# Kernel tuning notes

Hardware: AMD Instinct MI355X
Metric: run time of the kernel (lower is better)

The kernel has to match this reference:

```python
import jax, jax.numpy as jnp
import numpy as np

NEG = -1e9


def _layer_norm(x, g, b, eps=1e-5):
    m = x.mean(-1, keepdims=True)
    v = x.var(-1, keepdims=True)
    return (x - m) / jnp.sqrt(v + eps) * g + b


def _gat(x, mask, W, a):
    # x: [B,N,Fin], W: [Fin,Fout], a: [2*Fout]
    h = x @ W                                   # [B,N,Fout]
    F = W.shape[1]
    src = h @ a[:F]                             # [B,N]
    dst = h @ a[F:]                             # [B,N]
    e = jax.nn.leaky_relu(src[:, :, None] + dst[:, None, :], 0.2)  # [B,N,N]
    e = jnp.where(mask, e, NEG)
    attn = jax.nn.softmax(e, axis=-1)
    return attn @ h, attn


def _mha(x, mask, Wq, bq, Wk, bk, Wv, bv, Wo, bo, num_heads, head_dim):
    B, N, _ = x.shape
    q = (x @ Wq + bq).reshape(B, N, num_heads, head_dim)
    k = (x @ Wk + bk).reshape(B, N, num_heads, head_dim)
    v = (x @ Wv + bv).reshape(B, N, num_heads, head_dim)
    scores = jnp.einsum('bihd,bjhd->bhij', q, k) / jnp.sqrt(jnp.asarray(head_dim, x.dtype))
    scores = jnp.where(mask[:, None, :, :], scores, NEG)
    attn = jax.nn.softmax(scores, axis=-1)      # [B,H,N,N]
    ctx = jnp.einsum('bhij,bjhd->bihd', attn, v).reshape(B, N, num_heads * head_dim)
    return ctx @ Wo + bo, attn


def setup_inputs() -> dict:
    key = jax.random.key(0)
    ks = jax.random.split(key, 32)
    B, N = 64, 400
    D, Hd, E, H = 400, 256, 128, 4
    hd = Hd // H  # 64
    s = 0.02
    x = jax.random.normal(ks[0], (B, N, D), dtype=jnp.float32)
    adj = (jax.random.uniform(ks[1], (B, N, N)) < 0.15).astype(jnp.float32)
    eye = jnp.eye(N, dtype=jnp.float32)
    adj = jnp.maximum(adj, eye[None])
    def w(k, shape):
        return jax.random.normal(k, shape, dtype=jnp.float32) * s
    return {
        'x': x, 'adj': adj,
        'Wq': w(ks[2], (D, H * hd)), 'bq': jnp.zeros(H * hd),
        'Wk': w(ks[3], (D, H * hd)), 'bk': jnp.zeros(H * hd),
        'Wv': w(ks[4], (D, H * hd)), 'bv': jnp.zeros(H * hd),
        'Wo': w(ks[5], (H * hd, D)), 'bo': jnp.zeros(D),
        'gat1_W': w(ks[6], (D, Hd)), 'gat1_a': w(ks[7], (2 * Hd,)),
        'gat2_W': w(ks[8], (Hd, Hd)), 'gat2_a': w(ks[9], (2 * Hd,)),
        'gat3_W': w(ks[10], (Hd, E)), 'gat3_a': w(ks[11], (2 * E,)),
        'res1_W': w(ks[12], (D, Hd)), 'res1_b': jnp.zeros(Hd),
        'res2_W': w(ks[13], (Hd, Hd)), 'res2_b': jnp.zeros(Hd),
        'res3_W': w(ks[14], (Hd, E)), 'res3_b': jnp.zeros(E),
        'ln1_g': jnp.ones(Hd), 'ln1_b': jnp.zeros(Hd),
        'ln2_g': jnp.ones(Hd), 'ln2_b': jnp.zeros(Hd),
        'ln3_g': jnp.ones(E), 'ln3_b': jnp.zeros(E),
    }


def reference(x, adj, Wq, bq, Wk, bk, Wv, bv, Wo, bo,
              gat1_W, gat1_a, gat2_W, gat2_a, gat3_W, gat3_a,
              res1_W, res1_b, res2_W, res2_b, res3_W, res3_b,
              ln1_g, ln1_b, ln2_g, ln2_b, ln3_g, ln3_b):
    mask = adj > 0
    # eval mode: dropout is identity
    mha_out, _ = _mha(x, mask, Wq, bq, Wk, bk, Wv, bv, Wo, bo, num_heads=4, head_dim=64)
    x = x + mha_out
    g1, attn1 = _gat(x, mask, gat1_W, gat1_a)
    x = jax.nn.elu(_layer_norm(g1 + (x @ res1_W + res1_b), ln1_g, ln1_b))
    g2, attn2 = _gat(x, mask, gat2_W, gat2_a)
    x = jax.nn.elu(_layer_norm(g2 + (x @ res2_W + res2_b), ln2_g, ln2_b))
    g3, attn3 = _gat(x, mask, gat3_W, gat3_a)
    x = _layer_norm(g3 + (x @ res3_W + res3_b), ln3_g, ln3_b)
    return x, (attn1, attn2, attn3)
```

## Files before the change

kernel.cpp:

```cpp
#include <hip/hip_runtime.h>


#define NEGBIG (-1e9f)

typedef __attribute__((ext_vector_type(8))) short bf16x8;
typedef __attribute__((ext_vector_type(4))) float f32x4;

__device__ inline unsigned short f2bf(float f) {
    unsigned u = __builtin_bit_cast(unsigned, f);
    u += 0x7fffu + ((u >> 16) & 1u);
    return (unsigned short)(u >> 16);
}
__device__ inline float bf2f(unsigned short h) {
    unsigned u = ((unsigned)h) << 16;
    return __builtin_bit_cast(float, u);
}

__device__ inline float wave_max(float v) {
#pragma unroll
    for (int off = 32; off >= 1; off >>= 1)
        v = fmaxf(v, __shfl_xor(v, off, 64));
    return v;
}
__device__ inline float wave_sum(float v) {
#pragma unroll
    for (int off = 32; off >= 1; off >>= 1)
        v += __shfl_xor(v, off, 64);
    return v;
}

__global__ __launch_bounds__(256) void transpose_to_bf16(
    const float* __restrict__ in, unsigned short* __restrict__ out,
    int R, int C, long sIn, long sOut)
{
    in  += (long)blockIdx.z * sIn;
    out += (long)blockIdx.z * sOut;
    __shared__ float t[32][33];
    const int r0 = blockIdx.y * 32, c0 = blockIdx.x * 32;
    const int tid = threadIdx.x;

    const int row = tid >> 3, c4 = tid & 7;
    float4 v = make_float4(0.f, 0.f, 0.f, 0.f);
    if (r0 + row < R && c0 + c4 * 4 < C)
        v = *reinterpret_cast<const float4*>(&in[(long)(r0 + row) * C + c0 + c4 * 4]);
    t[row][c4 * 4 + 0] = v.x;
    t[row][c4 * 4 + 1] = v.y;
    t[row][c4 * 4 + 2] = v.z;
    t[row][c4 * 4 + 3] = v.w;
    __syncthreads();

    const int oc = tid >> 3, r4 = tid & 7;
    if (c0 + oc < C && r0 + r4 * 4 < R) {
        ushort4 o;
        o.x = f2bf(t[r4 * 4 + 0][oc]);
        o.y = f2bf(t[r4 * 4 + 1][oc]);
        o.z = f2bf(t[r4 * 4 + 2][oc]);
        o.w = f2bf(t[r4 * 4 + 3][oc]);
        *reinterpret_cast<ushort4*>(&out[(long)(c0 + oc) * R + r0 + r4 * 4]) = o;
    }
}

template<bool BIAS, bool ACCUM, bool RESID>
__global__ __launch_bounds__(256) void gemm_mfma(
    const float* __restrict__ A, const unsigned short* __restrict__ BT,
    const float* __restrict__ bias, const float* __restrict__ resid,
    float* __restrict__ C, int M, int K, int Nc,
    long sA, long sBT, long sC)
{
    const int bz = blockIdx.z;
    A  += (long)bz * sA;
    BT += (long)bz * sBT;
    C  += (long)bz * sC;
    const float* Rp = RESID ? (resid + (long)bz * sC) : nullptr;

    __shared__ short As[64][40];
    __shared__ short Bs[128][40];

    const int tid = threadIdx.x;
    const int lane = tid & 63, wave = tid >> 6;
    const int wm = wave >> 1, wn = wave & 1;
    const int m0 = blockIdx.y * 64, n0 = blockIdx.x * 128;

    f32x4 acc[2][4] = {};

    const int nk = (K + 31) / 32;
    for (int kt = 0; kt < nk; ++kt) {
        const int k0 = kt * 32;
        __syncthreads();
#pragma unroll
        for (int p = 0; p < 2; ++p) {
            const int idx = tid + p * 256;
            const int row = idx >> 3, k4 = idx & 7;
            const int gm = m0 + row, gk = k0 + k4 * 4;
            float4 av = make_float4(0.f, 0.f, 0.f, 0.f);
            if (gm < M && gk < K)
                av = *reinterpret_cast<const float4*>(&A[(long)gm * K + gk]);
            ushort4 h4;
            h4.x = f2bf(av.x); h4.y = f2bf(av.y); h4.z = f2bf(av.z); h4.w = f2bf(av.w);
            *reinterpret_cast<ushort4*>(&As[row][k4 * 4]) = h4;
        }
#pragma unroll
        for (int p = 0; p < 2; ++p) {
            const int idx = tid + p * 256;
            const int n = idx >> 2, k8 = idx & 3;
            const int gn = n0 + n, gk = k0 + k8 * 8;
            uint4 bv = make_uint4(0u, 0u, 0u, 0u);
            if (gn < Nc && gk < K)
                bv = *reinterpret_cast<const uint4*>(&BT[(long)gn * K + gk]);
            *reinterpret_cast<uint4*>(&Bs[n][k8 * 8]) = bv;
        }
        __syncthreads();

        const int fr = lane & 15, fkb = (lane >> 4) * 8;
        bf16x8 a[2], b[4];
#pragma unroll
        for (int i = 0; i < 2; ++i)
            a[i] = *reinterpret_cast<const bf16x8*>(&As[wm * 32 + i * 16 + fr][fkb]);
#pragma unroll
        for (int j = 0; j < 4; ++j)
            b[j] = *reinterpret_cast<const bf16x8*>(&Bs[wn * 64 + j * 16 + fr][fkb]);
#pragma unroll
        for (int i = 0; i < 2; ++i)
#pragma unroll
            for (int j = 0; j < 4; ++j)
                acc[i][j] = __builtin_amdgcn_mfma_f32_16x16x32_bf16(a[i], b[j], acc[i][j], 0, 0, 0);
    }

    const int fr = lane & 15, rg = lane >> 4;
#pragma unroll
    for (int i = 0; i < 2; ++i) {
#pragma unroll
        for (int j = 0; j < 4; ++j) {
#pragma unroll
            for (int r = 0; r < 4; ++r) {
                const int gm = m0 + wm * 32 + i * 16 + rg * 4 + r;
                const int gn = n0 + wn * 64 + j * 16 + fr;
                if (gm < M && gn < Nc) {
                    float v = acc[i][j][r];
                    if (BIAS)  v += bias[gn];
                    if (RESID) v += Rp[(long)gm * Nc + gn];
                    if (ACCUM) v += C[(long)gm * Nc + gn];
                    C[(long)gm * Nc + gn] = v;
                }
            }
        }
    }
}

__global__ __launch_bounds__(256) void mha_flash_mfma(
    const float* __restrict__ q, const float* __restrict__ k,
    const float* __restrict__ v, const float* __restrict__ adj,
    float* __restrict__ ctx)
{
    const int it = blockIdx.x, h = blockIdx.y, b = blockIdx.z;
    const int i0 = it * 64;
    const int tid = threadIdx.x;
    const int lane = tid & 63, w = tid >> 6;
    const int c = lane & 15, g = lane >> 4;

    __shared__ short Qs[64][72];
    __shared__ short Ks[64][72];
    __shared__ short Vt[64][72];
    __shared__ short Ps[64][72];
    __shared__ short Adjs[64][72];

    const long base_q = ((long)b * 400 + i0) * 256 + h * 64;
#pragma unroll
    for (int p = 0; p < 4; ++p) {
        const int idx = tid + p * 256;
        const int r = idx >> 4, c4 = idx & 15;
        float4 qv = make_float4(0.f, 0.f, 0.f, 0.f);
        if (i0 + r < 400)
            qv = *reinterpret_cast<const float4*>(q + base_q + (long)r * 256 + c4 * 4);
        ushort4 h4;
        h4.x = f2bf(qv.x); h4.y = f2bf(qv.y); h4.z = f2bf(qv.z); h4.w = f2bf(qv.w);
        *reinterpret_cast<ushort4*>(&Qs[r][c4 * 4]) = h4;
    }

    f32x4 o[4] = {};
    float m[4] = {-3e38f, -3e38f, -3e38f, -3e38f};
    float l[4] = {0.f, 0.f, 0.f, 0.f};

    for (int jt = 0; jt < 7; ++jt) {
        const int j0 = jt * 64;
        __syncthreads();

        const long base_k = ((long)b * 400 + j0) * 256 + h * 64;
#pragma unroll
        for (int p = 0; p < 4; ++p) {
            const int idx = tid + p * 256;
            const int r = idx >> 4, c4 = idx & 15;
            float4 kv = make_float4(0.f, 0.f, 0.f, 0.f);
            if (j0 + r < 400)
                kv = *reinterpret_cast<const float4*>(k + base_k + (long)r * 256 + c4 * 4);
            ushort4 h4;
            h4.x = f2bf(kv.x); h4.y = f2bf(kv.y); h4.z = f2bf(kv.z); h4.w = f2bf(kv.w);
            *reinterpret_cast<ushort4*>(&Ks[r][c4 * 4]) = h4;

            float4 av = make_float4(0.f, 0.f, 0.f, 0.f);
            if (i0 + r < 400 && j0 + c4 * 4 < 400)
                av = *reinterpret_cast<const float4*>(adj + ((long)b * 400 + i0 + r) * 400 + j0 + c4 * 4);
            ushort4 mb;
            mb.x = f2bf(av.x > 0.f ? 0.f : NEGBIG);
            mb.y = f2bf(av.y > 0.f ? 0.f : NEGBIG);
            mb.z = f2bf(av.z > 0.f ? 0.f : NEGBIG);
            mb.w = f2bf(av.w > 0.f ? 0.f : NEGBIG);
            *reinterpret_cast<ushort4*>(&Adjs[r][c4 * 4]) = mb;
        }
        {
            const int j4 = tid >> 4, d4 = tid & 15;
            float vv[4][4];
#pragma unroll
            for (int t = 0; t < 4; ++t) {
                float4 vl = make_float4(0.f, 0.f, 0.f, 0.f);
                if (j0 + j4 * 4 + t < 400)
                    vl = *reinterpret_cast<const float4*>(v + base_k + (long)(j4 * 4 + t) * 256 + d4 * 4);
                vv[t][0] = vl.x; vv[t][1] = vl.y; vv[t][2] = vl.z; vv[t][3] = vl.w;
            }
#pragma unroll
            for (int u = 0; u < 4; ++u) {
                ushort4 h4;
                h4.x = f2bf(vv[0][u]); h4.y = f2bf(vv[1][u]);
                h4.z = f2bf(vv[2][u]); h4.w = f2bf(vv[3][u]);
                *reinterpret_cast<ushort4*>(&Vt[d4 * 4 + u][j4 * 4]) = h4;
            }
        }
        __syncthreads();

        f32x4 s4[4] = {};
#pragma unroll
        for (int ks = 0; ks < 2; ++ks) {
            const bf16x8 a = *reinterpret_cast<const bf16x8*>(&Qs[w * 16 + c][ks * 32 + g * 8]);
#pragma unroll
            for (int t = 0; t < 4; ++t) {
                const bf16x8 bb = *reinterpret_cast<const bf16x8*>(&Ks[t * 16 + c][ks * 32 + g * 8]);
                s4[t] = __builtin_amdgcn_mfma_f32_16x16x32_bf16(a, bb, s4[t], 0, 0, 0);
            }
        }

        float e[4][4];
        float pmax[4];
#pragma unroll
        for (int reg = 0; reg < 4; ++reg) {
            const int qr = w * 16 + g * 4 + reg;
            float mx = -3e38f;
#pragma unroll
            for (int t = 0; t < 4; ++t) {
                const float ev = s4[t][reg] * 0.125f + bf2f((unsigned short)Adjs[qr][t * 16 + c]);
                e[t][reg] = ev;
                mx = fmaxf(mx, ev);
            }
            pmax[reg] = mx;
        }
#pragma unroll
        for (int reg = 0; reg < 4; ++reg)
#pragma unroll
            for (int off = 1; off <= 8; off <<= 1)
                pmax[reg] = fmaxf(pmax[reg], __shfl_xor(pmax[reg], off, 64));

        float al[4];
#pragma unroll
        for (int reg = 0; reg < 4; ++reg) {
            const float mn = fmaxf(m[reg], pmax[reg]);
            al[reg] = __expf(m[reg] - mn);
            m[reg] = mn;
        }

#pragma unroll
        for (int reg = 0; reg < 4; ++reg) {
            const int qr = w * 16 + g * 4 + reg;
            float psum = 0.f;
#pragma unroll
            for (int t = 0; t < 4; ++t) {
                const float p = __expf(e[t][reg] - m[reg]);
                psum += p;
                Ps[qr][t * 16 + c] = (short)f2bf(p);
            }
            l[reg] = l[reg] * al[reg] + psum;
        }

#pragma unroll
        for (int dt = 0; dt < 4; ++dt)
#pragma unroll
            for (int reg = 0; reg < 4; ++reg)
                o[dt][reg] *= al[reg];

#pragma unroll
        for (int ks = 0; ks < 2; ++ks) {
            const bf16x8 a = *reinterpret_cast<const bf16x8*>(&Ps[w * 16 + c][ks * 32 + g * 8]);
#pragma unroll
            for (int dt = 0; dt < 4; ++dt) {
                const bf16x8 bb = *reinterpret_cast<const bf16x8*>(&Vt[dt * 16 + c][ks * 32 + g * 8]);
                o[dt] = __builtin_amdgcn_mfma_f32_16x16x32_bf16(a, bb, o[dt], 0, 0, 0);
            }
        }
    }

#pragma unroll
    for (int reg = 0; reg < 4; ++reg)
#pragma unroll
        for (int off = 1; off <= 8; off <<= 1)
            l[reg] += __shfl_xor(l[reg], off, 64);

#pragma unroll
    for (int reg = 0; reg < 4; ++reg) {
        const int gi = i0 + w * 16 + g * 4 + reg;
        if (gi < 400) {
            const float inv = 1.f / l[reg];
#pragma unroll
            for (int dt = 0; dt < 4; ++dt)
                ctx[((long)b * 400 + gi) * 256 + h * 64 + dt * 16 + c] = o[dt][reg] * inv;
        }
    }
}

__global__ __launch_bounds__(256) void gat_srcdst(
    const float* __restrict__ h, const float* __restrict__ a,
    float* __restrict__ src, float* __restrict__ dst, int F)
{
    const int row = blockIdx.x * 4 + (threadIdx.x >> 6);
    const int lane = threadIdx.x & 63;
    const float* hp = h + (long)row * F;
    float s = 0.f, d = 0.f;
    for (int f = lane; f < F; f += 64) {
        const float hv = hp[f];
        s += hv * a[f];
        d += hv * a[F + f];
    }
    s = wave_sum(s);
    d = wave_sum(d);
    if (lane == 0) { src[row] = s; dst[row] = d; }
}

__global__ __launch_bounds__(256) void gat_attn(
    const float* __restrict__ src, const float* __restrict__ dst,
    const float* __restrict__ adj, float* __restrict__ attn)
{
    const int row = blockIdx.x * 4 + (threadIdx.x >> 6);
    const int b = row / 400;
    const int lane = threadIdx.x & 63;
    const float si = src[row];
    const float* db = dst + (long)b * 400;
    const float* adjrow = adj + (long)row * 400;

    float e[7];
    float mx = -3.0e38f;
#pragma unroll
    for (int t = 0; t < 7; ++t) {
        const int j = lane + 64 * t;
        float v = -3.0e38f;
        if (j < 400) {
            v = si + db[j];
            v = (v > 0.f) ? v : 0.2f * v;
            if (!(adjrow[j] > 0.f)) v = NEGBIG;
        }
        e[t] = v;
        mx = fmaxf(mx, v);
    }
    mx = wave_max(mx);

    float p[7];
    float sum = 0.f;
#pragma unroll
    for (int t = 0; t < 7; ++t) {
        const int j = lane + 64 * t;
        if (j < 400) {
            p[t] = __expf(e[t] - mx);
            sum += p[t];
        }
    }
    sum = wave_sum(sum);
    const float inv = 1.f / sum;
#pragma unroll
    for (int t = 0; t < 7; ++t) {
        const int j = lane + 64 * t;
        if (j < 400) attn[(long)row * 400 + j] = p[t] * inv;
    }
}

template<int F, bool ELU>
__global__ __launch_bounds__(256) void ln_kernel(
    const float* __restrict__ in, const float* __restrict__ g,
    const float* __restrict__ b, float* __restrict__ out)
{
    const int row = blockIdx.x * 4 + (threadIdx.x >> 6);
    const int lane = threadIdx.x & 63;
    constexpr int PER = F / 64;
    const float* ip = in + (long)row * F;

    float v[PER];
    float s = 0.f;
#pragma unroll
    for (int t = 0; t < PER; ++t) {
        v[t] = ip[lane + 64 * t];
        s += v[t];
    }
    s = wave_sum(s);
    const float mean = s * (1.f / F);
    float vs = 0.f;
#pragma unroll
    for (int t = 0; t < PER; ++t) {
        const float d = v[t] - mean;
        vs += d * d;
    }
    vs = wave_sum(vs);
    const float rstd = rsqrtf(vs * (1.f / F) + 1e-5f);
#pragma unroll
    for (int t = 0; t < PER; ++t) {
        const int col = lane + 64 * t;
        float y = (v[t] - mean) * rstd * g[col] + b[col];
        if (ELU) y = (y > 0.f) ? y : expm1f(y);
        out[(long)row * F + col] = y;
    }
}

extern "C" void kernel_launch(void* const* d_in, const int* in_sizes, int n_in,
                              void* d_out, int out_size, void* d_ws, size_t ws_size,
                              hipStream_t stream) {
    const float* x    = (const float*)d_in[0];
    const float* adj  = (const float*)d_in[1];
    const float* Wq   = (const float*)d_in[2];
    const float* bq   = (const float*)d_in[3];
    const float* Wk   = (const float*)d_in[4];
    const float* bk   = (const float*)d_in[5];
    const float* Wv   = (const float*)d_in[6];
    const float* bv   = (const float*)d_in[7];
    const float* Wo   = (const float*)d_in[8];
    const float* bo   = (const float*)d_in[9];
    const float* g1W  = (const float*)d_in[10];
    const float* g1a  = (const float*)d_in[11];
    const float* g2W  = (const float*)d_in[12];
    const float* g2a  = (const float*)d_in[13];
    const float* g3W  = (const float*)d_in[14];
    const float* g3a  = (const float*)d_in[15];
    const float* r1W  = (const float*)d_in[16];
    const float* r1b  = (const float*)d_in[17];
    const float* r2W  = (const float*)d_in[18];
    const float* r2b  = (const float*)d_in[19];
    const float* r3W  = (const float*)d_in[20];
    const float* r3b  = (const float*)d_in[21];
    const float* ln1g = (const float*)d_in[22];
    const float* ln1b = (const float*)d_in[23];
    const float* ln2g = (const float*)d_in[24];
    const float* ln2b = (const float*)d_in[25];
    const float* ln3g = (const float*)d_in[26];
    const float* ln3b = (const float*)d_in[27];

    float* out_x = (float*)d_out;
    float* attn1 = out_x + 3276800;
    float* attn2 = attn1 + 10240000;
    float* attn3 = attn2 + 10240000;

    float* bufA = (float*)d_ws;
    float* bufB = bufA + 6553600;
    float* bufC = bufB + 6553600;
    float* bufD = bufC + 6553600;
    float* srcb = bufD + 6553600;
    float* dstb = srcb + 25600;
    unsigned short* wT   = (unsigned short*)(dstb + 25600);
    unsigned short* wTq  = wT;
    unsigned short* wTk  = wT + 102400;
    unsigned short* wTv  = wT + 204800;
    unsigned short* wTo  = wT + 307200;
    unsigned short* wTg1 = wT + 409600;
    unsigned short* wTr1 = wT + 512000;
    unsigned short* wTg2 = wT + 614400;
    unsigned short* wTr2 = wT + 679936;
    unsigned short* wTg3 = wT + 745472;
    unsigned short* wTr3 = wT + 778240;
    float* xc = attn1;
    unsigned short* hT1 = (unsigned short*)bufD;
    unsigned short* hT2 = (unsigned short*)bufC;
    unsigned short* hT3 = (unsigned short*)bufD;

    const dim3 blk(256);
    const int M = 25600;

    transpose_to_bf16<<<dim3(8, 13), blk, 0, stream>>>(Wq,  wTq, 400, 256, 0, 0);
    transpose_to_bf16<<<dim3(8, 13), blk, 0, stream>>>(Wk,  wTk, 400, 256, 0, 0);
    transpose_to_bf16<<<dim3(8, 13), blk, 0, stream>>>(Wv,  wTv, 400, 256, 0, 0);
    transpose_to_bf16<<<dim3(13, 8), blk, 0, stream>>>(Wo,  wTo, 256, 400, 0, 0);
    transpose_to_bf16<<<dim3(8, 13), blk, 0, stream>>>(g1W, wTg1, 400, 256, 0, 0);
    transpose_to_bf16<<<dim3(8, 13), blk, 0, stream>>>(r1W, wTr1, 400, 256, 0, 0);
    transpose_to_bf16<<<dim3(8, 8),  blk, 0, stream>>>(g2W, wTg2, 256, 256, 0, 0);
    transpose_to_bf16<<<dim3(8, 8),  blk, 0, stream>>>(r2W, wTr2, 256, 256, 0, 0);
    transpose_to_bf16<<<dim3(4, 8),  blk, 0, stream>>>(g3W, wTg3, 256, 128, 0, 0);
    transpose_to_bf16<<<dim3(4, 8),  blk, 0, stream>>>(r3W, wTr3, 256, 128, 0, 0);

    gemm_mfma<true, false, false><<<dim3(2, 400), blk, 0, stream>>>(x, wTq, bq, nullptr, bufA, M, 400, 256, 0, 0, 0);
    gemm_mfma<true, false, false><<<dim3(2, 400), blk, 0, stream>>>(x, wTk, bk, nullptr, bufB, M, 400, 256, 0, 0, 0);
    gemm_mfma<true, false, false><<<dim3(2, 400), blk, 0, stream>>>(x, wTv, bv, nullptr, bufC, M, 400, 256, 0, 0, 0);
    mha_flash_mfma<<<dim3(7, 4, 64), blk, 0, stream>>>(bufA, bufB, bufC, adj, bufD);
    gemm_mfma<true, false, true><<<dim3(4, 400), blk, 0, stream>>>(bufD, wTo, bo, x, xc, M, 256, 400, 0, 0, 0);

    gemm_mfma<false, false, false><<<dim3(2, 400), blk, 0, stream>>>(xc, wTg1, nullptr, nullptr, bufA, M, 400, 256, 0, 0, 0);
    gemm_mfma<true, false, false><<<dim3(2, 400), blk, 0, stream>>>(xc, wTr1, r1b, nullptr, bufB, M, 400, 256, 0, 0, 0);
    gat_srcdst<<<dim3(6400), blk, 0, stream>>>(bufA, g1a, srcb, dstb, 256);
    gat_attn<<<dim3(6400), blk, 0, stream>>>(srcb, dstb, adj, attn1);
    transpose_to_bf16<<<dim3(8, 13, 64), blk, 0, stream>>>(bufA, hT1, 400, 256, 102400, 102400);
    gemm_mfma<false, true, false><<<dim3(2, 7, 64), blk, 0, stream>>>(attn1, hT1, nullptr, nullptr, bufB, 400, 400, 256, 160000, 102400, 102400);
    ln_kernel<256, true><<<dim3(6400), blk, 0, stream>>>(bufB, ln1g, ln1b, bufD);

    gemm_mfma<false, false, false><<<dim3(2, 400), blk, 0, stream>>>(bufD, wTg2, nullptr, nullptr, bufA, M, 256, 256, 0, 0, 0);
    gemm_mfma<true, false, false><<<dim3(2, 400), blk, 0, stream>>>(bufD, wTr2, r2b, nullptr, bufB, M, 256, 256, 0, 0, 0);
    gat_srcdst<<<dim3(6400), blk, 0, stream>>>(bufA, g2a, srcb, dstb, 256);
    gat_attn<<<dim3(6400), blk, 0, stream>>>(srcb, dstb, adj, attn2);
    transpose_to_bf16<<<dim3(8, 13, 64), blk, 0, stream>>>(bufA, hT2, 400, 256, 102400, 102400);
    gemm_mfma<false, true, false><<<dim3(2, 7, 64), blk, 0, stream>>>(attn2, hT2, nullptr, nullptr, bufB, 400, 400, 256, 160000, 102400, 102400);
    ln_kernel<256, true><<<dim3(6400), blk, 0, stream>>>(bufB, ln2g, ln2b, bufC);

    gemm_mfma<false, false, false><<<dim3(1, 400), blk, 0, stream>>>(bufC, wTg3, nullptr, nullptr, bufA, M, 256, 128, 0, 0, 0);
    gemm_mfma<true, false, false><<<dim3(1, 400), blk, 0, stream>>>(bufC, wTr3, r3b, nullptr, bufB, M, 256, 128, 0, 0, 0);
    gat_srcdst<<<dim3(6400), blk, 0, stream>>>(bufA, g3a, srcb, dstb, 128);
    gat_attn<<<dim3(6400), blk, 0, stream>>>(srcb, dstb, adj, attn3);
    transpose_to_bf16<<<dim3(4, 13, 64), blk, 0, stream>>>(bufA, hT3, 400, 128, 51200, 51200);
    gemm_mfma<false, true, false><<<dim3(1, 7, 64), blk, 0, stream>>>(attn3, hT3, nullptr, nullptr, bufB, 400, 400, 128, 160000, 51200, 51200);
    ln_kernel<128, false><<<dim3(6400), blk, 0, stream>>>(bufB, ln3g, ln3b, out_x);
}
```

Measured before the change: 882.4 us.

## Fuse QKV and GAT/residual projection GEMMs and enlarge GEMM tiles to 128x256

Result: faster. 852.3 us (-3.4%).

```diff
diff --git a/kernel.cpp b/kernel.cpp
--- a/kernel.cpp
+++ b/kernel.cpp
@@ -29,9 +29,21 @@
     return v;
 }
 
+__global__ void build_biases(
+    float* bqkv, const float* bq, const float* bk, const float* bv,
+    float* bgr1, const float* r1b, float* bgr2, const float* r2b,
+    float* bgr3, const float* r3b)
+{
+    const int t = threadIdx.x;
+    bqkv[t] = bq[t]; bqkv[256 + t] = bk[t]; bqkv[512 + t] = bv[t];
+    bgr1[t] = 0.f; bgr1[256 + t] = r1b[t];
+    bgr2[t] = 0.f; bgr2[256 + t] = r2b[t];
+    if (t < 128) { bgr3[t] = 0.f; bgr3[128 + t] = r3b[t]; }
+}
+
 __global__ __launch_bounds__(256) void transpose_to_bf16(
     const float* __restrict__ in, unsigned short* __restrict__ out,
-    int R, int C, long sIn, long sOut)
+    int R, int C, int ldIn, long sIn, long sOut)
 {
     in  += (long)blockIdx.z * sIn;
     out += (long)blockIdx.z * sOut;
@@ -42,7 +54,7 @@
     const int row = tid >> 3, c4 = tid & 7;
     float4 v = make_float4(0.f, 0.f, 0.f, 0.f);
     if (r0 + row < R && c0 + c4 * 4 < C)
-        v = *reinterpret_cast<const float4*>(&in[(long)(r0 + row) * C + c0 + c4 * 4]);
+        v = *reinterpret_cast<const float4*>(&in[(long)(r0 + row) * ldIn + c0 + c4 * 4]);
     t[row][c4 * 4 + 0] = v.x;
     t[row][c4 * 4 + 1] = v.y;
     t[row][c4 * 4 + 2] = v.z;
@@ -61,10 +73,10 @@
 }
 
 template<bool BIAS, bool ACCUM, bool RESID>
-__global__ __launch_bounds__(256) void gemm_mfma(
+__global__ __launch_bounds__(512) void gemm_mfma(
     const float* __restrict__ A, const unsigned short* __restrict__ BT,
     const float* __restrict__ bias, const float* __restrict__ resid,
-    float* __restrict__ C, int M, int K, int Nc,
+    float* __restrict__ C, int M, int K, int Nc, int ldA, int ldC,
     long sA, long sBT, long sC)
 {
     const int bz = blockIdx.z;
@@ -73,15 +85,15 @@
     C  += (long)bz * sC;
     const float* Rp = RESID ? (resid + (long)bz * sC) : nullptr;
 
-    __shared__ short As[64][40];
-    __shared__ short Bs[128][40];
+    __shared__ short As[128][40];
+    __shared__ short Bs[256][40];
 
     const int tid = threadIdx.x;
     const int lane = tid & 63, wave = tid >> 6;
-    const int wm = wave >> 1, wn = wave & 1;
-    const int m0 = blockIdx.y * 64, n0 = blockIdx.x * 128;
-
-    f32x4 acc[2][4] = {};
+    const int wm = wave >> 2, wn = wave & 3;
+    const int m0 = blockIdx.y * 128, n0 = blockIdx.x * 256;
+
+    f32x4 acc[4][4] = {};
 
     const int nk = (K + 31) / 32;
     for (int kt = 0; kt < nk; ++kt) {
@@ -89,19 +101,19 @@
         __syncthreads();
 #pragma unroll
         for (int p = 0; p < 2; ++p) {
-            const int idx = tid + p * 256;
+            const int idx = tid + p * 512;
             const int row = idx >> 3, k4 = idx & 7;
             const int gm = m0 + row, gk = k0 + k4 * 4;
             float4 av = make_float4(0.f, 0.f, 0.f, 0.f);
             if (gm < M && gk < K)
-                av = *reinterpret_cast<const float4*>(&A[(long)gm * K + gk]);
+                av = *reinterpret_cast<const float4*>(&A[(long)gm * ldA + gk]);
             ushort4 h4;
             h4.x = f2bf(av.x); h4.y = f2bf(av.y); h4.z = f2bf(av.z); h4.w = f2bf(av.w);
             *reinterpret_cast<ushort4*>(&As[row][k4 * 4]) = h4;
         }
 #pragma unroll
         for (int p = 0; p < 2; ++p) {
-            const int idx = tid + p * 256;
+            const int idx = tid + p * 512;
             const int n = idx >> 2, k8 = idx & 3;
             const int gn = n0 + n, gk = k0 + k8 * 8;
             uint4 bv = make_uint4(0u, 0u, 0u, 0u);
@@ -112,15 +124,15 @@
         __syncthreads();
 
         const int fr = lane & 15, fkb = (lane >> 4) * 8;
-        bf16x8 a[2], b[4];
-#pragma unroll
-        for (int i = 0; i < 2; ++i)
-            a[i] = *reinterpret_cast<const bf16x8*>(&As[wm * 32 + i * 16 + fr][fkb]);
+        bf16x8 a[4], b[4];
+#pragma unroll
+        for (int i = 0; i < 4; ++i)
+            a[i] = *reinterpret_cast<const bf16x8*>(&As[wm * 64 + i * 16 + fr][fkb]);
 #pragma unroll
         for (int j = 0; j < 4; ++j)
             b[j] = *reinterpret_cast<const bf16x8*>(&Bs[wn * 64 + j * 16 + fr][fkb]);
 #pragma unroll
-        for (int i = 0; i < 2; ++i)
+        for (int i = 0; i < 4; ++i)
 #pragma unroll
             for (int j = 0; j < 4; ++j)
                 acc[i][j] = __builtin_amdgcn_mfma_f32_16x16x32_bf16(a[i], b[j], acc[i][j], 0, 0, 0);
@@ -128,19 +140,19 @@
 
     const int fr = lane & 15, rg = lane >> 4;
 #pragma unroll
-    for (int i = 0; i < 2; ++i) {
+    for (int i = 0; i < 4; ++i) {
 #pragma unroll
         for (int j = 0; j < 4; ++j) {
 #pragma unroll
             for (int r = 0; r < 4; ++r) {
-                const int gm = m0 + wm * 32 + i * 16 + rg * 4 + r;
+                const int gm = m0 + wm * 64 + i * 16 + rg * 4 + r;
                 const int gn = n0 + wn * 64 + j * 16 + fr;
                 if (gm < M && gn < Nc) {
                     float v = acc[i][j][r];
                     if (BIAS)  v += bias[gn];
-                    if (RESID) v += Rp[(long)gm * Nc + gn];
-                    if (ACCUM) v += C[(long)gm * Nc + gn];
-                    C[(long)gm * Nc + gn] = v;
+                    if (RESID) v += Rp[(long)gm * ldC + gn];
+                    if (ACCUM) v += C[(long)gm * ldC + gn];
+                    C[(long)gm * ldC + gn] = v;
                 }
             }
         }
@@ -148,9 +160,8 @@
 }
 
 __global__ __launch_bounds__(256) void mha_flash_mfma(
-    const float* __restrict__ q, const float* __restrict__ k,
-    const float* __restrict__ v, const float* __restrict__ adj,
-    float* __restrict__ ctx)
+    const float* __restrict__ qkv, const float* __restrict__ adj,
+    float* __restrict__ ctx, int ld)
 {
     const int it = blockIdx.x, h = blockIdx.y, b = blockIdx.z;
     const int i0 = it * 64;
@@ -164,14 +175,14 @@
     __shared__ short Ps[64][72];
     __shared__ short Adjs[64][72];
 
-    const long base_q = ((long)b * 400 + i0) * 256 + h * 64;
+    const long base_q = ((long)b * 400 + i0) * ld + h * 64;
 #pragma unroll
     for (int p = 0; p < 4; ++p) {
         const int idx = tid + p * 256;
         const int r = idx >> 4, c4 = idx & 15;
         float4 qv = make_float4(0.f, 0.f, 0.f, 0.f);
         if (i0 + r < 400)
-            qv = *reinterpret_cast<const float4*>(q + base_q + (long)r * 256 + c4 * 4);
+            qv = *reinterpret_cast<const float4*>(qkv + base_q + (long)r * ld + c4 * 4);
         ushort4 h4;
         h4.x = f2bf(qv.x); h4.y = f2bf(qv.y); h4.z = f2bf(qv.z); h4.w = f2bf(qv.w);
         *reinterpret_cast<ushort4*>(&Qs[r][c4 * 4]) = h4;
@@ -185,14 +196,15 @@
         const int j0 = jt * 64;
         __syncthreads();
 
-        const long base_k = ((long)b * 400 + j0) * 256 + h * 64;
+        const long base_k = ((long)b * 400 + j0) * ld + 256 + h * 64;
+        const long base_v = base_k + 256;
 #pragma unroll
         for (int p = 0; p < 4; ++p) {
             const int idx = tid + p * 256;
             const int r = idx >> 4, c4 = idx & 15;
             float4 kv = make_float4(0.f, 0.f, 0.f, 0.f);
             if (j0 + r < 400)
-                kv = *reinterpret_cast<const float4*>(k + base_k + (long)r * 256 + c4 * 4);
+                kv = *reinterpret_cast<const float4*>(qkv + base_k + (long)r * ld + c4 * 4);
             ushort4 h4;
             h4.x = f2bf(kv.x); h4.y = f2bf(kv.y); h4.z = f2bf(kv.z); h4.w = f2bf(kv.w);
             *reinterpret_cast<ushort4*>(&Ks[r][c4 * 4]) = h4;
@@ -214,7 +226,7 @@
             for (int t = 0; t < 4; ++t) {
                 float4 vl = make_float4(0.f, 0.f, 0.f, 0.f);
                 if (j0 + j4 * 4 + t < 400)
-                    vl = *reinterpret_cast<const float4*>(v + base_k + (long)(j4 * 4 + t) * 256 + d4 * 4);
+                    vl = *reinterpret_cast<const float4*>(qkv + base_v + (long)(j4 * 4 + t) * ld + d4 * 4);
                 vv[t][0] = vl.x; vv[t][1] = vl.y; vv[t][2] = vl.z; vv[t][3] = vl.w;
             }
 #pragma unroll
@@ -316,11 +328,11 @@
 
 __global__ __launch_bounds__(256) void gat_srcdst(
     const float* __restrict__ h, const float* __restrict__ a,
-    float* __restrict__ src, float* __restrict__ dst, int F)
+    float* __restrict__ src, float* __restrict__ dst, int F, int ld)
 {
     const int row = blockIdx.x * 4 + (threadIdx.x >> 6);
     const int lane = threadIdx.x & 63;
-    const float* hp = h + (long)row * F;
+    const float* hp = h + (long)row * ld;
     float s = 0.f, d = 0.f;
     for (int f = lane; f < F; f += 64) {
         const float hv = hp[f];
@@ -380,13 +392,13 @@
 
 template<int F, bool ELU>
 __global__ __launch_bounds__(256) void ln_kernel(
-    const float* __restrict__ in, const float* __restrict__ g,
+    const float* __restrict__ in, int ldIn, const float* __restrict__ g,
     const float* __restrict__ b, float* __restrict__ out)
 {
     const int row = blockIdx.x * 4 + (threadIdx.x >> 6);
     const int lane = threadIdx.x & 63;
     constexpr int PER = F / 64;
-    const float* ip = in + (long)row * F;
+    const float* ip = in + (long)row * ldIn;
 
     float v[PER];
     float s = 0.f;
@@ -468,52 +480,66 @@
     unsigned short* wTr2 = wT + 679936;
     unsigned short* wTg3 = wT + 745472;
     unsigned short* wTr3 = wT + 778240;
-    float* xc = attn1;
-    unsigned short* hT1 = (unsigned short*)bufD;
-    unsigned short* hT2 = (unsigned short*)bufC;
-    unsigned short* hT3 = (unsigned short*)bufD;
-
-    const dim3 blk(256);
+    float* bias0 = (float*)(wT + 811008);
+    float* bqkv = bias0;
+    float* bgr1 = bqkv + 768;
+    float* bgr2 = bgr1 + 512;
+    float* bgr3 = bgr2 + 512;
+
+    float* qkv = bufA;
+    float* ctx = bufD;
+    float* xc  = attn1;
+    float* hr1 = bufA;
+    float* hr3 = bufA;
+    unsigned short* hT = (unsigned short*)bufD;
+    float* x2 = bufC;
+    float* x3 = bufC;
+
+    const dim3 b256(256), b512(512);
     const int M = 25600;
 
-    transpose_to_bf16<<<dim3(8, 13), blk, 0, stream>>>(Wq,  wTq, 400, 256, 0, 0);
-    transpose_to_bf16<<<dim3(8, 13), blk, 0, stream>>>(Wk,  wTk, 400, 256, 0, 0);
-    transpose_to_bf16<<<dim3(8, 13), blk, 0, stream>>>(Wv,  wTv, 400, 256, 0, 0);
-    transpose_to_bf16<<<dim3(13, 8), blk, 0, stream>>>(Wo,  wTo, 256, 400, 0, 0);
-    transpose_to_bf16<<<dim3(8, 13), blk, 0, stream>>>(g1W, wTg1, 400, 256, 0, 0);
-    transpose_to_bf16<<<dim3(8, 13), blk, 0, stream>>>(r1W, wTr1, 400, 256, 0, 0);
-    transpose_to_bf16<<<dim3(8, 8),  blk, 0, stream>>>(g2W, wTg2, 256, 256, 0, 0);
-    transpose_to_bf16<<<dim3(8, 8),  blk, 0, stream>>>(r2W, wTr2, 256, 256, 0, 0);
-    transpose_to_bf16<<<dim3(4, 8),  blk, 0, stream>>>(g3W, wTg3, 256, 128, 0, 0);
-    transpose_to_bf16<<<dim3(4, 8),  blk, 0, stream>>>(r3W, wTr3, 256, 128, 0, 0);
-
-    gemm_mfma<true, false, false><<<dim3(2, 400), blk, 0, stream>>>(x, wTq, bq, nullptr, bufA, M, 400, 256, 0, 0, 0);
-    gemm_mfma<true, false, false><<<dim3(2, 400), blk, 0, stream>>>(x, wTk, bk, nullptr, bufB, M, 400, 256, 0, 0, 0);
-    gemm_mfma<true, false, false><<<dim3(2, 400), blk, 0, stream>>>(x, wTv, bv, nullptr, bufC, M, 400, 256, 0, 0, 0);
-    mha_flash_mfma<<<dim3(7, 4, 64), blk, 0, stream>>>(bufA, bufB, bufC, adj, bufD);
-    gemm_mfma<true, false, true><<<dim3(4, 400), blk, 0, stream>>>(bufD, wTo, bo, x, xc, M, 256, 400, 0, 0, 0);
-
-    gemm_mfma<false, false, false><<<dim3(2, 400), blk, 0, stream>>>(xc, wTg1, nullptr, nullptr, bufA, M, 400, 256, 0, 0, 0);
-    gemm_mfma<true, false, false><<<dim3(2, 400), blk, 0, stream>>>(xc, wTr1, r1b, nullptr, bufB, M, 400, 256, 0, 0, 0);
-    gat_srcdst<<<dim3(6400), blk, 0, stream>>>(bufA, g1a, srcb, dstb, 256);
-    gat_attn<<<dim3(6400), blk, 0, stream>>>(srcb, dstb, adj, attn1);
-    transpose_to_bf16<<<dim3(8, 13, 64), blk, 0, stream>>>(bufA, hT1, 400, 256, 102400, 102400);
-    gemm_mfma<false, true, false><<<dim3(2, 7, 64), blk, 0, stream>>>(attn1, hT1, nullptr, nullptr, bufB, 400, 400, 256, 160000, 102400, 102400);
-    ln_kernel<256, true><<<dim3(6400), blk, 0, stream>>>(bufB, ln1g, ln1b, bufD);
-
-    gemm_mfma<false, false, false><<<dim3(2, 400), blk, 0, stream>>>(bufD, wTg2, nullptr, nullptr, bufA, M, 256, 256, 0, 0, 0);
-    gemm_mfma<true, false, false><<<dim3(2, 400), blk, 0, stream>>>(bufD, wTr2, r2b, nullptr, bufB, M, 256, 256, 0, 0, 0);
-    gat_srcdst<<<dim3(6400), blk, 0, stream>>>(bufA, g2a, srcb, dstb, 256);
-    gat_attn<<<dim3(6400), blk, 0, stream>>>(srcb, dstb, adj, attn2);
-    transpose_to_bf16<<<dim3(8, 13, 64), blk, 0, stream>>>(bufA, hT2, 400, 256, 102400, 102400);
-    gemm_mfma<false, true, false><<<dim3(2, 7, 64), blk, 0, stream>>>(attn2, hT2, nullptr, nullptr, bufB, 400, 400, 256, 160000, 102400, 102400);
-    ln_kernel<256, true><<<dim3(6400), blk, 0, stream>>>(bufB, ln2g, ln2b, bufC);
-
-    gemm_mfma<false, false, false><<<dim3(1, 400), blk, 0, stream>>>(bufC, wTg3, nullptr, nullptr, bufA, M, 256, 128, 0, 0, 0);
-    gemm_mfma<true, false, false><<<dim3(1, 400), blk, 0, stream>>>(bufC, wTr3, r3b, nullptr, bufB, M, 256, 128, 0, 0, 0);
-    gat_srcdst<<<dim3(6400), blk, 0, stream>>>(bufA, g3a, srcb, dstb, 128);
-    gat_attn<<<dim3(6400), blk, 0, stream>>>(srcb, dstb, adj, attn3);
-    transpose_to_bf16<<<dim3(4, 13, 64), blk, 0, stream>>>(bufA, hT3, 400, 128, 51200, 51200);
-    gemm_mfma<false, true, false><<<dim3(1, 7, 64), blk, 0, stream>>>(attn3, hT3, nullptr, nullptr, bufB, 400, 400, 128, 160000, 51200, 51200);
-    ln_kernel<128, false><<<dim3(6400), blk, 0, stream>>>(bufB, ln3g, ln3b, out_x);
-}
+    build_biases<<<1, b256, 0, stream>>>(bqkv, bq, bk, bv, bgr1, r1b, bgr2, r2b, bgr3, r3b);
+    transpose_to_bf16<<<dim3(8, 13), b256, 0, stream>>>(Wq,  wTq, 400, 256, 256, 0, 0);
+    transpose_to_bf16<<<dim3(8, 13), b256, 0, stream>>>(Wk,  wTk, 400, 256, 256, 0, 0);
+    transpose_to_bf16<<<dim3(8, 13), b256, 0, stream>>>(Wv,  wTv, 400, 256, 256, 0, 0);
+    transpose_to_bf16<<<dim3(13, 8), b256, 0, stream>>>(Wo,  wTo, 256, 400, 400, 0, 0);
+    transpose_to_bf16<<<dim3(8, 13), b256, 0, stream>>>(g1W, wTg1, 400, 256, 256, 0, 0);
+    transpose_to_bf16<<<dim3(8, 13), b256, 0, stream>>>(r1W, wTr1, 400, 256, 256, 0, 0);
+    transpose_to_bf16<<<dim3(8, 8),  b256, 0, stream>>>(g2W, wTg2, 256, 256, 256, 0, 0);
+    transpose_to_bf16<<<dim3(8, 8),  b256, 0, stream>>>(r2W, wTr2, 256, 256, 256, 0, 0);
+    transpose_to_bf16<<<dim3(4, 8),  b256, 0, stream>>>(g3W, wTg3, 256, 128, 128, 0, 0);
+    transpose_to_bf16<<<dim3(4, 8),  b256, 0, stream>>>(r3W, wTr3, 256, 128, 128, 0, 0);
+
+    gemm_mfma<true, false, false><<<dim3(3, 200), b512, 0, stream>>>(
+        x, wTq, bqkv, nullptr, qkv, M, 400, 768, 400, 768, 0, 0, 0);
+    mha_flash_mfma<<<dim3(7, 4, 64), b256, 0, stream>>>(qkv, adj, ctx, 768);
+    gemm_mfma<true, false, true><<<dim3(2, 200), b512, 0, stream>>>(
+        ctx, wTo, bo, x, xc, M, 256, 400, 256, 400, 0, 0, 0);
+
+    gemm_mfma<true, false, false><<<dim3(2, 200), b512, 0, stream>>>(
+        xc, wTg1, bgr1, nullptr, hr1, M, 400, 512, 400, 512, 0, 0, 0);
+    gat_srcdst<<<dim3(6400), b256, 0, stream>>>(hr1, g1a, srcb, dstb, 256, 512);
+    gat_attn<<<dim3(6400), b256, 0, stream>>>(srcb, dstb, adj, attn1);
+    transpose_to_bf16<<<dim3(8, 13, 64), b256, 0, stream>>>(hr1, hT, 400, 256, 512, 204800, 102400);
+    gemm_mfma<false, true, false><<<dim3(1, 4, 64), b512, 0, stream>>>(
+        attn1, hT, nullptr, nullptr, hr1 + 256, 400, 400, 256, 400, 512, 160000, 102400, 204800);
+    ln_kernel<256, true><<<dim3(6400), b256, 0, stream>>>(hr1 + 256, 512, ln1g, ln1b, x2);
+
+    gemm_mfma<true, false, false><<<dim3(2, 200), b512, 0, stream>>>(
+        x2, wTg2, bgr2, nullptr, hr1, M, 256, 512, 256, 512, 0, 0, 0);
+    gat_srcdst<<<dim3(6400), b256, 0, stream>>>(hr1, g2a, srcb, dstb, 256, 512);
+    gat_attn<<<dim3(6400), b256, 0, stream>>>(srcb, dstb, adj, attn2);
+    transpose_to_bf16<<<dim3(8, 13, 64), b256, 0, stream>>>(hr1, hT, 400, 256, 512, 204800, 102400);
+    gemm_mfma<false, true, false><<<dim3(1, 4, 64), b512, 0, stream>>>(
+        attn2, hT, nullptr, nullptr, hr1 + 256, 400, 400, 256, 400, 512, 160000, 102400, 204800);
+    ln_kernel<256, true><<<dim3(6400), b256, 0, stream>>>(hr1 + 256, 512, ln2g, ln2b, x3);
+
+    gemm_mfma<true, false, false><<<dim3(1, 200), b512, 0, stream>>>(
+        x3, wTg3, bgr3, nullptr, hr3, M, 256, 256, 256, 256, 0, 0, 0);
+    gat_srcdst<<<dim3(6400), b256, 0, stream>>>(hr3, g3a, srcb, dstb, 128, 256);
+    gat_attn<<<dim3(6400), b256, 0, stream>>>(srcb, dstb, adj, attn3);
+    transpose_to_bf16<<<dim3(4, 13, 64), b256, 0, stream>>>(hr3, hT, 400, 128, 256, 102400, 51200);
+    gemm_mfma<false, true, false><<<dim3(1, 4, 64), b512, 0, stream>>>(
+        attn3, hT, nullptr, nullptr, hr3 + 128, 400, 400, 128, 400, 256, 160000, 51200, 102400);
+    ln_kernel<128, false><<<dim3(6400), b256, 0, stream>>>(hr3 + 128, 256, ln3g, ln3b, out_x);
+}
```
